# Optimization experiments

Measured on AMD Instinct MI355X. Metric: run time of the kernel, lower is better.

Reference implementation:

```python
import jax, jax.numpy as jnp
import numpy as np

NPOS_MAX = 64
SCALE = 0.125  # head_dim ** -0.5


def setup_inputs() -> dict:
    key = jax.random.key(0)
    kq, kk, kv, kp, kw = jax.random.split(key, 5)
    B, S, D = 32, 1024, 64
    return {
        "q": jax.random.normal(kq, (B, S, D), dtype=jnp.float32),
        "k": jax.random.normal(kk, (B, S, D), dtype=jnp.float32),
        "v": jax.random.normal(kv, (B, S, D), dtype=jnp.float32),
        "pos_emb": jax.random.normal(kp, (1, D, NPOS_MAX), dtype=jnp.float32) * 0.02,
        "w_k": jax.random.normal(kw, (1, D, D), dtype=jnp.float32) * 0.02,
        "is_cope_k": 1,
    }


def reference(q, k, v, pos_emb, w_k, is_cope_k):
    # mode == 0: plain scaled QK^T
    attn_logits = jnp.einsum("bqd,bkd->bqk", q * SCALE, k)  # [B,S,S]
    gates = jax.nn.sigmoid(attn_logits)
    # reverse cumulative sum along the key axis (flip-cumsum-flip)
    pos = jnp.cumsum(gates[..., ::-1], axis=-1)[..., ::-1]
    pos = jnp.minimum(pos, NPOS_MAX - 1)
    pos_ceil = jnp.ceil(pos).astype(jnp.int32)
    pos_floor = jnp.floor(pos).astype(jnp.int32)
    base = q if is_cope_k else k
    logits_int = jnp.einsum("bsd,odn->bsn", base, pos_emb)  # [B,S,npos]
    logits_ceil = jnp.take_along_axis(logits_int, pos_ceil, axis=-1)
    logits_floor = jnp.take_along_axis(logits_int, pos_floor, axis=-1)
    w = pos - pos_floor.astype(pos.dtype)
    return logits_ceil * w + logits_floor * (1.0 - w)
```

## Files before the change

kernel.cpp:

```cpp
#include <hip/hip_runtime.h>


#define SLEN 1024
#define DDIM 64
#define NPOS 64
#define QROWS 16
#define QCOLS 256
#define COPE_SCALE 0.125f
#define GSTR 260
#define TSTR 66

typedef __bf16 bf16x8 __attribute__((ext_vector_type(8)));
typedef float f32x4 __attribute__((ext_vector_type(4)));

__device__ __forceinline__ unsigned short f2bf_hi(float x) {
    unsigned u = __builtin_bit_cast(unsigned, x);
    unsigned r = u + 0x7FFFu + ((u >> 16) & 1u);
    return (unsigned short)(r >> 16);
}
__device__ __forceinline__ float bf2f(unsigned short h) {
    unsigned u = ((unsigned)h) << 16;
    return __builtin_bit_cast(float, u);
}
struct U8 { ushort4 a, b; };
__device__ __forceinline__ bf16x8 pack8(const unsigned short* s) {
    U8 u = {{s[0], s[1], s[2], s[3]}, {s[4], s[5], s[6], s[7]}};
    return __builtin_bit_cast(bf16x8, u);
}

__device__ __forceinline__ void load_split16(const float* __restrict__ row,
                                             bf16x8* hi, bf16x8* lo) {
    #pragma unroll
    for (int ks = 0; ks < 2; ++ks) {
        float4 v0 = *(const float4*)(row + ks * 32);
        float4 v1 = *(const float4*)(row + ks * 32 + 4);
        float xs[8] = {v0.x, v0.y, v0.z, v0.w, v1.x, v1.y, v1.z, v1.w};
        unsigned short hb[8], lb[8];
        #pragma unroll
        for (int j = 0; j < 8; ++j) {
            hb[j] = f2bf_hi(xs[j]);
            lb[j] = f2bf_hi(xs[j] - bf2f(hb[j]));
        }
        hi[ks] = pack8(hb);
        lo[ks] = pack8(lb);
    }
}

__global__ __launch_bounds__(256, 6) void cope_mfma_kernel(
    const float* __restrict__ q,
    const float* __restrict__ k,
    const float* __restrict__ pos_emb,
    const int*   __restrict__ is_cope_k,
    float*       __restrict__ out)
{
    __shared__ __align__(16) float G[QROWS * GSTR];
    __shared__ __align__(16) float tableL[QROWS * TSTR];
    __shared__ float Racc[QROWS];

    const int t = threadIdx.x;
    const int wave = t >> 6;
    const int lane = t & 63;
    const int quad = lane >> 4;
    const int nloc = lane & 15;

    const int nwg = gridDim.x;
    const int phys = blockIdx.x;
    const int blk = ((nwg & 7) == 0) ? ((phys & 7) * (nwg >> 3) + (phys >> 3))
                                     : phys;
    const int batch = blk >> 6;
    const int qbase = (blk & 63) * QROWS;

    if (t < QROWS) Racc[t] = 0.f;

    bf16x8 a_hi[2], a_lo[2];
    load_split16(q + (size_t)(batch * SLEN + qbase + nloc) * DDIM + quad * 8,
                 a_hi, a_lo);

    {
        const int icope = *is_cope_k;
        bf16x8 t_hi[2], t_lo[2];
        if (icope) {
            t_hi[0] = a_hi[0]; t_hi[1] = a_hi[1];
            t_lo[0] = a_lo[0]; t_lo[1] = a_lo[1];
        } else {
            load_split16(k + (size_t)(batch * SLEN + qbase + nloc) * DDIM + quad * 8,
                         t_hi, t_lo);
        }
        bf16x8 p_hi[2];
        #pragma unroll
        for (int ks = 0; ks < 2; ++ks) {
            unsigned short hb[8];
            #pragma unroll
            for (int j = 0; j < 8; ++j) {
                float pv = pos_emb[(quad * 8 + j + ks * 32) * NPOS + wave * 16 + nloc];
                hb[j] = f2bf_hi(pv);
            }
            p_hi[ks] = pack8(hb);
        }
        f32x4 tacc = {0.f, 0.f, 0.f, 0.f};
        tacc = __builtin_amdgcn_mfma_f32_16x16x32_bf16(t_hi[0], p_hi[0], tacc, 0, 0, 0);
        tacc = __builtin_amdgcn_mfma_f32_16x16x32_bf16(t_lo[0], p_hi[0], tacc, 0, 0, 0);
        tacc = __builtin_amdgcn_mfma_f32_16x16x32_bf16(t_hi[1], p_hi[1], tacc, 0, 0, 0);
        tacc = __builtin_amdgcn_mfma_f32_16x16x32_bf16(t_lo[1], p_hi[1], tacc, 0, 0, 0);
        #pragma unroll
        for (int reg = 0; reg < 4; ++reg)
            tableL[(quad * 4 + reg) * TSTR + wave * 16 + nloc] = tacc[reg];
    }
    __syncthreads();

    #pragma unroll
    for (int rep = 0; rep < 4; ++rep) {
        const int row = wave * 4 + rep;
        const float v63 = tableL[row * TSTR + (NPOS - 1)];
        f32x4 bv = {v63, v63, v63, v63};
        float* orow = out + (size_t)(batch * SLEN + qbase + row) * SLEN;
        #pragma unroll
        for (int c = 0; c < 3; ++c)
            __builtin_nontemporal_store(bv, (f32x4*)(orow + c * QCOLS + lane * 4));
    }

    for (int qi = 3; qi >= 0; --qi) {
        #pragma unroll
        for (int i = 0; i < 4; ++i) {
            const int tl = wave * 4 + i;
            const float* krow =
                k + (size_t)(batch * SLEN + qi * QCOLS + tl * 16 + nloc) * DDIM + quad * 8;
            bf16x8 bh[2], bl[2];
            load_split16(krow, bh, bl);
            f32x4 acc = {0.f, 0.f, 0.f, 0.f};
            acc = __builtin_amdgcn_mfma_f32_16x16x32_bf16(a_hi[0], bh[0], acc, 0, 0, 0);
            acc = __builtin_amdgcn_mfma_f32_16x16x32_bf16(a_lo[0], bh[0], acc, 0, 0, 0);
            acc = __builtin_amdgcn_mfma_f32_16x16x32_bf16(a_hi[0], bl[0], acc, 0, 0, 0);
            acc = __builtin_amdgcn_mfma_f32_16x16x32_bf16(a_hi[1], bh[1], acc, 0, 0, 0);
            acc = __builtin_amdgcn_mfma_f32_16x16x32_bf16(a_lo[1], bh[1], acc, 0, 0, 0);
            acc = __builtin_amdgcn_mfma_f32_16x16x32_bf16(a_hi[1], bl[1], acc, 0, 0, 0);
            #pragma unroll
            for (int reg = 0; reg < 4; ++reg) {
                float x = acc[reg] * COPE_SCALE;
                float g = __builtin_amdgcn_rcpf(1.0f + __expf(-x));
                G[(quad * 4 + reg) * GSTR + tl * 16 + nloc] = g;
            }
        }
        __syncthreads();

        #pragma unroll
        for (int rep = 0; rep < 4; ++rep) {
            const int row = wave * 4 + rep;
            const float roff = Racc[row];
            float4 gv = *(const float4*)&G[row * GSTR + lane * 4];
            float ls3 = gv.w;
            float ls2 = gv.z + ls3;
            float ls1 = gv.y + ls2;
            float ls0 = gv.x + ls1;
            const float T = ls0;
            float v = T;
            #pragma unroll
            for (int ofs = 1; ofs < 64; ofs <<= 1) {
                float u = __shfl_down(v, ofs);
                if (lane + ofs < 64) v += u;
            }
            if (lane == 0) Racc[row] = roff + v;
            const float E = (v - T) + roff;

            const float tabv = tableL[row * TSTR + lane];
            float dtabv = __shfl_down(tabv, 1) - tabv;
            if (lane == 63) dtabv = 0.f;
            float ls[4] = {ls0, ls1, ls2, ls3};
            float res[4];
            #pragma unroll
            for (int i = 0; i < 4; ++i) {
                float p = ls[i] + E;
                p = fminf(p, (float)(NPOS - 1));
                float pf = floorf(p);
                int fi = (int)pf;
                float w = p - pf;
                float tf = __shfl(tabv, fi);
                float td = __shfl(dtabv, fi);
                res[i] = tf + w * td;
            }
            float* orow = out + (size_t)(batch * SLEN + qbase + row) * SLEN + qi * QCOLS + lane * 4;
            f32x4 o = {res[0], res[1], res[2], res[3]};
            __builtin_nontemporal_store(o, (f32x4*)orow);
        }
        __syncthreads();

        float mn = Racc[0];
        #pragma unroll
        for (int r = 1; r < QROWS; ++r) mn = fminf(mn, Racc[r]);
        if (mn >= (float)(NPOS - 1)) break;
    }
}

extern "C" void kernel_launch(void* const* d_in, const int* in_sizes, int n_in,
                              void* d_out, int out_size, void* d_ws, size_t ws_size,
                              hipStream_t stream) {
    (void)n_in; (void)out_size; (void)d_ws; (void)ws_size;
    const float* q         = (const float*)d_in[0];
    const float* k         = (const float*)d_in[1];
    const float* pos_emb   = (const float*)d_in[3];
    const int*   is_cope_k = (const int*)d_in[5];
    float* out = (float*)d_out;

    const int B = in_sizes[0] / (SLEN * DDIM);
    cope_mfma_kernel<<<B * (SLEN / QROWS), 256, 0, stream>>>(
        q, k, pos_emb, is_cope_k, out);
}
```

Measured before the change: 184.4 us.

## Precompute bf16 hi/lo split of late K tiles in workspace and reorder phases

Adds a prep kernel that converts the second half of each batch's K rows into bf16 hi/lo pairs in the workspace. The main kernel then loads those pairs directly for the first two key chunks it processes, instead of redoing the split in every one of the 64 blocks that share a batch. It also moves the first QK^T/sigmoid chunk ahead of the positional-table MFMA and the constant-fill stores, so that early global loads can overlap with that work. The cost is an extra kernel launch and extra workspace reads and writes.

```diff
diff --git a/kernel.cpp b/kernel.cpp
--- a/kernel.cpp
+++ b/kernel.cpp
@@ -46,11 +46,36 @@
     }
 }
 
+__global__ __launch_bounds__(256) void prep_kernel(
+    const float* __restrict__ k,
+    unsigned short* __restrict__ khi,
+    unsigned short* __restrict__ klo,
+    int n4h)
+{
+    int j = blockIdx.x * 256 + threadIdx.x;
+    if (j >= n4h) return;
+    const int HB4 = (SLEN / 2) * DDIM / 4;
+    int batch = j / HB4;
+    int rem   = j - batch * HB4;
+    int i = batch * (SLEN * DDIM / 4) + HB4 + rem;
+    float4 v = ((const float4*)k)[i];
+    ushort4 h, l;
+    h.x = f2bf_hi(v.x); l.x = f2bf_hi(v.x - bf2f(h.x));
+    h.y = f2bf_hi(v.y); l.y = f2bf_hi(v.y - bf2f(h.y));
+    h.z = f2bf_hi(v.z); l.z = f2bf_hi(v.z - bf2f(h.z));
+    h.w = f2bf_hi(v.w); l.w = f2bf_hi(v.w - bf2f(h.w));
+    ((ushort4*)khi)[i] = h;
+    ((ushort4*)klo)[i] = l;
+}
+
 __global__ __launch_bounds__(256, 6) void cope_mfma_kernel(
     const float* __restrict__ q,
     const float* __restrict__ k,
     const float* __restrict__ pos_emb,
     const int*   __restrict__ is_cope_k,
+    const unsigned short* __restrict__ khi,
+    const unsigned short* __restrict__ klo,
+    int ws_ok,
     float*       __restrict__ out)
 {
     __shared__ __align__(16) float G[QROWS * GSTR];
@@ -76,57 +101,21 @@
     load_split16(q + (size_t)(batch * SLEN + qbase + nloc) * DDIM + quad * 8,
                  a_hi, a_lo);
 
-    {
-        const int icope = *is_cope_k;
-        bf16x8 t_hi[2], t_lo[2];
-        if (icope) {
-            t_hi[0] = a_hi[0]; t_hi[1] = a_hi[1];
-            t_lo[0] = a_lo[0]; t_lo[1] = a_lo[1];
-        } else {
-            load_split16(k + (size_t)(batch * SLEN + qbase + nloc) * DDIM + quad * 8,
-                         t_hi, t_lo);
-        }
-        bf16x8 p_hi[2];
-        #pragma unroll
-        for (int ks = 0; ks < 2; ++ks) {
-            unsigned short hb[8];
-            #pragma unroll
-            for (int j = 0; j < 8; ++j) {
-                float pv = pos_emb[(quad * 8 + j + ks * 32) * NPOS + wave * 16 + nloc];
-                hb[j] = f2bf_hi(pv);
-            }
-            p_hi[ks] = pack8(hb);
-        }
-        f32x4 tacc = {0.f, 0.f, 0.f, 0.f};
-        tacc = __builtin_amdgcn_mfma_f32_16x16x32_bf16(t_hi[0], p_hi[0], tacc, 0, 0, 0);
-        tacc = __builtin_amdgcn_mfma_f32_16x16x32_bf16(t_lo[0], p_hi[0], tacc, 0, 0, 0);
-        tacc = __builtin_amdgcn_mfma_f32_16x16x32_bf16(t_hi[1], p_hi[1], tacc, 0, 0, 0);
-        tacc = __builtin_amdgcn_mfma_f32_16x16x32_bf16(t_lo[1], p_hi[1], tacc, 0, 0, 0);
-        #pragma unroll
-        for (int reg = 0; reg < 4; ++reg)
-            tableL[(quad * 4 + reg) * TSTR + wave * 16 + nloc] = tacc[reg];
-    }
-    __syncthreads();
-
-    #pragma unroll
-    for (int rep = 0; rep < 4; ++rep) {
-        const int row = wave * 4 + rep;
-        const float v63 = tableL[row * TSTR + (NPOS - 1)];
-        f32x4 bv = {v63, v63, v63, v63};
-        float* orow = out + (size_t)(batch * SLEN + qbase + row) * SLEN;
-        #pragma unroll
-        for (int c = 0; c < 3; ++c)
-            __builtin_nontemporal_store(bv, (f32x4*)(orow + c * QCOLS + lane * 4));
-    }
-
-    for (int qi = 3; qi >= 0; --qi) {
+    auto phaseB = [&](int qi, bool use_ws) {
         #pragma unroll
         for (int i = 0; i < 4; ++i) {
             const int tl = wave * 4 + i;
-            const float* krow =
-                k + (size_t)(batch * SLEN + qi * QCOLS + tl * 16 + nloc) * DDIM + quad * 8;
+            const size_t boff =
+                (size_t)(batch * SLEN + qi * QCOLS + tl * 16 + nloc) * DDIM + quad * 8;
             bf16x8 bh[2], bl[2];
-            load_split16(krow, bh, bl);
+            if (use_ws) {
+                bh[0] = __builtin_bit_cast(bf16x8, *(const uint4*)(khi + boff));
+                bh[1] = __builtin_bit_cast(bf16x8, *(const uint4*)(khi + boff + 32));
+                bl[0] = __builtin_bit_cast(bf16x8, *(const uint4*)(klo + boff));
+                bl[1] = __builtin_bit_cast(bf16x8, *(const uint4*)(klo + boff + 32));
+            } else {
+                load_split16(k + boff, bh, bl);
+            }
             f32x4 acc = {0.f, 0.f, 0.f, 0.f};
             acc = __builtin_amdgcn_mfma_f32_16x16x32_bf16(a_hi[0], bh[0], acc, 0, 0, 0);
             acc = __builtin_amdgcn_mfma_f32_16x16x32_bf16(a_lo[0], bh[0], acc, 0, 0, 0);
@@ -141,8 +130,9 @@
                 G[(quad * 4 + reg) * GSTR + tl * 16 + nloc] = g;
             }
         }
-        __syncthreads();
-
+    };
+
+    auto phaseD = [&](int qi) {
         #pragma unroll
         for (int rep = 0; rep < 4; ++rep) {
             const int row = wave * 4 + rep;
@@ -182,8 +172,68 @@
             f32x4 o = {res[0], res[1], res[2], res[3]};
             __builtin_nontemporal_store(o, (f32x4*)orow);
         }
+    };
+
+    phaseB(3, ws_ok != 0);
+
+    {
+        const int icope = *is_cope_k;
+        bf16x8 t_hi[2], t_lo[2];
+        if (icope) {
+            t_hi[0] = a_hi[0]; t_hi[1] = a_hi[1];
+            t_lo[0] = a_lo[0]; t_lo[1] = a_lo[1];
+        } else {
+            load_split16(k + (size_t)(batch * SLEN + qbase + nloc) * DDIM + quad * 8,
+                         t_hi, t_lo);
+        }
+        bf16x8 p_hi[2];
+        #pragma unroll
+        for (int ks = 0; ks < 2; ++ks) {
+            unsigned short hb[8];
+            #pragma unroll
+            for (int j = 0; j < 8; ++j) {
+                float pv = pos_emb[(quad * 8 + j + ks * 32) * NPOS + wave * 16 + nloc];
+                hb[j] = f2bf_hi(pv);
+            }
+            p_hi[ks] = pack8(hb);
+        }
+        f32x4 tacc = {0.f, 0.f, 0.f, 0.f};
+        tacc = __builtin_amdgcn_mfma_f32_16x16x32_bf16(t_hi[0], p_hi[0], tacc, 0, 0, 0);
+        tacc = __builtin_amdgcn_mfma_f32_16x16x32_bf16(t_lo[0], p_hi[0], tacc, 0, 0, 0);
+        tacc = __builtin_amdgcn_mfma_f32_16x16x32_bf16(t_hi[1], p_hi[1], tacc, 0, 0, 0);
+        tacc = __builtin_amdgcn_mfma_f32_16x16x32_bf16(t_lo[1], p_hi[1], tacc, 0, 0, 0);
+        #pragma unroll
+        for (int reg = 0; reg < 4; ++reg)
+            tableL[(quad * 4 + reg) * TSTR + wave * 16 + nloc] = tacc[reg];
+    }
+    __syncthreads();
+
+    #pragma unroll
+    for (int rep = 0; rep < 4; ++rep) {
+        const int row = wave * 4 + rep;
+        const float v63 = tableL[row * TSTR + (NPOS - 1)];
+        f32x4 bv = {v63, v63, v63, v63};
+        float* orow = out + (size_t)(batch * SLEN + qbase + row) * SLEN;
+        #pragma unroll
+        for (int c = 0; c < 3; ++c)
+            __builtin_nontemporal_store(bv, (f32x4*)(orow + c * QCOLS + lane * 4));
+    }
+
+    phaseD(3);
+    __syncthreads();
+
+    {
+        float mn = Racc[0];
+        #pragma unroll
+        for (int r = 1; r < QROWS; ++r) mn = fminf(mn, Racc[r]);
+        if (mn >= (float)(NPOS - 1)) return;
+    }
+
+    for (int qi = 2; qi >= 0; --qi) {
+        phaseB(qi, ws_ok != 0 && qi >= 2);
         __syncthreads();
-
+        phaseD(qi);
+        __syncthreads();
         float mn = Racc[0];
         #pragma unroll
         for (int r = 1; r < QROWS; ++r) mn = fminf(mn, Racc[r]);
@@ -194,14 +244,25 @@
 extern "C" void kernel_launch(void* const* d_in, const int* in_sizes, int n_in,
                               void* d_out, int out_size, void* d_ws, size_t ws_size,
                               hipStream_t stream) {
-    (void)n_in; (void)out_size; (void)d_ws; (void)ws_size;
+    (void)n_in; (void)out_size;
     const float* q         = (const float*)d_in[0];
     const float* k         = (const float*)d_in[1];
     const float* pos_emb   = (const float*)d_in[3];
     const int*   is_cope_k = (const int*)d_in[5];
     float* out = (float*)d_out;
 
+    const int nk = in_sizes[1];
     const int B = in_sizes[0] / (SLEN * DDIM);
+    const size_t ws_need = (size_t)nk * 2 * sizeof(unsigned short);
+
+    unsigned short* khi = (unsigned short*)d_ws;
+    unsigned short* klo = khi + nk;
+    const int ws_ok = (ws_size >= ws_need) ? 1 : 0;
+
+    if (ws_ok) {
+        int n4h = nk / 8;
+        prep_kernel<<<(n4h + 255) / 256, 256, 0, stream>>>(k, khi, klo, n4h);
+    }
     cope_mfma_kernel<<<B * (SLEN / QROWS), 256, 0, stream>>>(
-        q, k, pos_emb, is_cope_k, out);
-}
+        q, k, pos_emb, is_cope_k, khi, klo, ws_ok, out);
+}
```

Result: faster. 178.8 us (-3.1%).
